# Optimization experiments

Measured on AMD Instinct MI355X. Metric: run time of the kernel, lower is better.

The kernel has to match this reference:

```python
import jax, jax.numpy as jnp
import numpy as np

N = 50000
EPS = 1e-16


def _gat_conv(x, w, att_src, att_dst, bias, src, dst, heads, out_ch, concat):
    # x: [N, F_in]; w: [heads*out_ch, F_in]; att_*: [heads, out_ch]; bias: [heads*out_ch] or [out_ch]
    n = x.shape[0]
    xw = (x @ w.T).reshape(n, heads, out_ch)              # [N, H, C]
    a_src = jnp.einsum('nhc,hc->nh', xw, att_src)          # [N, H]
    a_dst = jnp.einsum('nhc,hc->nh', xw, att_dst)
    alpha = a_src[src] + a_dst[dst]                        # [E, H]
    alpha = jax.nn.leaky_relu(alpha, negative_slope=0.2)
    # segment softmax over destination node (every node has a self loop)
    m = jax.ops.segment_max(alpha, dst, num_segments=n)    # [N, H]
    e = jnp.exp(alpha - m[dst])
    s = jax.ops.segment_sum(e, dst, num_segments=n)        # [N, H]
    coef = e / (s[dst] + EPS)                              # [E, H]
    out = jax.ops.segment_sum(xw[src] * coef[:, :, None], dst, num_segments=n)  # [N, H, C]
    if concat:
        out = out.reshape(n, heads * out_ch)
    else:
        out = out.mean(axis=1)
    return out + bias


def setup_inputs() -> dict:
    key = jax.random.key(0)
    ks = jax.random.split(key, 8)
    F_in, H, C1, NC = 128, 2, 64, 16
    E = 1_600_000
    x = jax.random.normal(ks[0], (N, F_in), dtype=jnp.float32)
    edge_index = jax.random.randint(ks[1], (2, E), 0, N, dtype=jnp.int64)
    w1 = jax.random.normal(ks[2], (H * C1, F_in), dtype=jnp.float32) / np.sqrt(F_in)
    att_src1 = jax.random.normal(ks[3], (H, C1), dtype=jnp.float32) / np.sqrt(C1)
    att_dst1 = jax.random.normal(ks[4], (H, C1), dtype=jnp.float32) / np.sqrt(C1)
    b1 = jnp.zeros((H * C1,), dtype=jnp.float32)
    w2 = jax.random.normal(ks[5], (NC, H * C1), dtype=jnp.float32) / np.sqrt(H * C1)
    att_src2 = jax.random.normal(ks[6], (1, NC), dtype=jnp.float32) / np.sqrt(NC)
    att_dst2 = jax.random.normal(ks[7], (1, NC), dtype=jnp.float32) / np.sqrt(NC)
    b2 = jnp.zeros((NC,), dtype=jnp.float32)
    return {"x": x, "edge_index": edge_index, "w1": w1, "att_src1": att_src1,
            "att_dst1": att_dst1, "b1": b1, "w2": w2, "att_src2": att_src2,
            "att_dst2": att_dst2, "b2": b2}


def reference(x, edge_index, w1, att_src1, att_dst1, b1, w2, att_src2, att_dst2, b2):
    n = x.shape[0]
    loop = jnp.arange(n, dtype=edge_index.dtype)
    src = jnp.concatenate([edge_index[0], loop])  # PyG adds self loops by default
    dst = jnp.concatenate([edge_index[1], loop])
    h = _gat_conv(x, w1, att_src1, att_dst1, b1, src, dst, heads=2, out_ch=64, concat=True)
    h = jax.nn.relu(h)
    # dropout p=0.5 is identity in eval mode
    out = _gat_conv(h, w2, att_src2, att_dst2, b2, src, dst, heads=1, out_ch=16, concat=True)
    return out
```

## Files before the change

kernel.cpp:

```cpp
#include <hip/hip_runtime.h>
#include <hip/hip_fp16.h>


#define BSHIFT 7
#define MAXB 512
#define CAPMAX 6144
#define XS 136

using f16x8 = __attribute__((ext_vector_type(8))) _Float16;
using f16x4 = __attribute__((ext_vector_type(4))) _Float16;
using f32x4 = __attribute__((ext_vector_type(4))) float;

__device__ __forceinline__ float lrelu(float a) { return fmaxf(a, 0.2f * a); }


__global__ __launch_bounds__(256) void part_gemm1_kernel(
    const int* __restrict__ src, const int* __restrict__ dst,
    int* __restrict__ bincur, unsigned* __restrict__ binned,
    int E, int B, int CH, int CAP, int NB,
    const float* __restrict__ x, const float* __restrict__ w1,
    const float* __restrict__ as1, const float* __restrict__ ad1,
    __half* __restrict__ xw1h, float* __restrict__ asrc1,
    float* __restrict__ adst1, int N) {
  __shared__ __align__(16) char smem[(64 + 128) * XS * 2];
  int t = threadIdx.x;

  if (blockIdx.x < (unsigned)NB) {
    int* s_h = (int*)smem;
    int* s_base = s_h + MAXB;
    int* s_cur = s_base + MAXB;
    unsigned* s_pack = (unsigned*)(s_cur + MAXB);
    for (int i = t; i < B; i += 256) s_h[i] = 0;
    __syncthreads();
    int lo = blockIdx.x * CH;
    int cnt = min(CH, E - lo);
    for (int i = t; i < cnt; i += 256) {
      int d = dst[lo + i];
      int s = src[lo + i];
      atomicAdd(&s_h[d >> BSHIFT], 1);
      s_pack[i] = (unsigned)s | ((unsigned)(d & 127) << 16) |
                  ((unsigned)(d >> BSHIFT) << 23);
    }
    __syncthreads();
    for (int i = t; i < B; i += 256) {
      int c = s_h[i];
      s_base[i] = c ? (i * CAP + atomicAdd(&bincur[i], c)) : 0;
      s_cur[i] = 0;
    }
    __syncthreads();
    for (int i = t; i < cnt; i += 256) {
      unsigned e = s_pack[i];
      int b = e >> 23;
      int r = atomicAdd(&s_cur[b], 1);
      binned[s_base[b] + r] = e & 0x7FFFFFu;
    }
    return;
  }

  _Float16* lx = (_Float16*)smem;
  _Float16* lw = lx + 64 * XS;
  int n0 = (blockIdx.x - NB) * 64;

#pragma unroll
  for (int j = 0; j < 8; ++j) {
    int idx = t + 256 * j;
    int nd = idx >> 5, i4 = (idx & 31) * 4;
    int gn = n0 + nd;
    float4 v = (gn < N) ? *(const float4*)&x[(size_t)gn * 128 + i4]
                        : make_float4(0.f, 0.f, 0.f, 0.f);
    f16x4 h;
    h[0] = (_Float16)v.x; h[1] = (_Float16)v.y;
    h[2] = (_Float16)v.z; h[3] = (_Float16)v.w;
    *(f16x4*)&lx[nd * XS + i4] = h;
  }
#pragma unroll
  for (int j = 0; j < 16; ++j) {
    int idx = t + 256 * j;
    int o = idx >> 5, i4 = (idx & 31) * 4;
    float4 v = *(const float4*)&w1[(size_t)o * 128 + i4];
    f16x4 h;
    h[0] = (_Float16)v.x; h[1] = (_Float16)v.y;
    h[2] = (_Float16)v.z; h[3] = (_Float16)v.w;
    *(f16x4*)&lw[o * XS + i4] = h;
  }
  __syncthreads();

  int lane = t & 63, wv = t >> 6;
  int m16 = lane & 15, q = lane >> 4;

  f32x4 acc[8];
#pragma unroll
  for (int i = 0; i < 8; ++i) acc[i] = (f32x4){0.f, 0.f, 0.f, 0.f};

#pragma unroll
  for (int c = 0; c < 4; ++c) {
    f16x8 a = *(const f16x8*)&lx[(16 * wv + m16) * XS + c * 32 + q * 8];
#pragma unroll
    for (int tt = 0; tt < 8; ++tt) {
      f16x8 b = *(const f16x8*)&lw[(tt * 16 + m16) * XS + c * 32 + q * 8];
      acc[tt] = __builtin_amdgcn_mfma_f32_16x16x32_f16(a, b, acc[tt], 0, 0, 0);
    }
  }

#pragma unroll
  for (int tt = 0; tt < 8; ++tt) {
#pragma unroll
    for (int r = 0; r < 4; ++r) {
      lx[(16 * wv + 4 * q + r) * XS + tt * 16 + m16] = (_Float16)acc[tt][r];
    }
  }

  {
    float ps = 0.f, pd = 0.f;
    int p = q;
#pragma unroll
    for (int k = 0; k < 4; ++k) {
      f16x8 hv = *(const f16x8*)&lx[(16 * wv + m16) * XS + p * 32 + k * 8];
      float4 s0 = *(const float4*)&as1[p * 32 + k * 8];
      float4 s1 = *(const float4*)&as1[p * 32 + k * 8 + 4];
      float4 d0 = *(const float4*)&ad1[p * 32 + k * 8];
      float4 d1 = *(const float4*)&ad1[p * 32 + k * 8 + 4];
      ps += (float)hv[0] * s0.x + (float)hv[1] * s0.y + (float)hv[2] * s0.z +
            (float)hv[3] * s0.w + (float)hv[4] * s1.x + (float)hv[5] * s1.y +
            (float)hv[6] * s1.z + (float)hv[7] * s1.w;
      pd += (float)hv[0] * d0.x + (float)hv[1] * d0.y + (float)hv[2] * d0.z +
            (float)hv[3] * d0.w + (float)hv[4] * d1.x + (float)hv[5] * d1.y +
            (float)hv[6] * d1.z + (float)hv[7] * d1.w;
    }
    ps += __shfl_xor(ps, 16);
    pd += __shfl_xor(pd, 16);
    int n = n0 + 16 * wv + m16;
    if (n < N && (q == 0 || q == 2)) {
      int hh = q >> 1;
      asrc1[2 * n + hh] = ps;
      adst1[2 * n + hh] = pd;
    }
  }

#pragma unroll
  for (int i = 0; i < 4; ++i) {
    int m = q + 4 * i;
    int n = n0 + 16 * wv + m;
    if (n < N) {
      uint4 v = *(const uint4*)&lx[(16 * wv + m) * XS + m16 * 8];
      *(uint4*)&xw1h[(size_t)n * 128 + m16 * 8] = v;
    }
  }
}


__global__ __launch_bounds__(256) void bucket_build_kernel(const unsigned* __restrict__ binned,
                                                           const int* __restrict__ bincur,
                                                           int2* __restrict__ nodeseg,
                                                           unsigned short* __restrict__ csr,
                                                           int N, int CAP) {
  __shared__ int s_deg[128];
  __shared__ int s_cur[128];
  __shared__ int s_wsum;
  __shared__ unsigned s_edges[CAPMAX];
  int b = blockIdx.x;
  int lo = b * CAP, hi = lo + bincur[b];
  int cnt = hi - lo;
  int t = threadIdx.x;
  if (t < 128) s_deg[t] = 0;
  int stg = min(cnt, CAPMAX);
  for (int i = t; i < stg; i += 256) s_edges[i] = binned[lo + i];
  __syncthreads();
  for (int i = t; i < cnt; i += 256) {
    unsigned e = (i < CAPMAX) ? s_edges[i] : binned[lo + i];
    atomicAdd(&s_deg[e >> 16], 1);
  }
  __syncthreads();
  int lane = t & 63, wv = t >> 6;
  int v = (t < 128) ? s_deg[t] : 0;
  int incl = v;
#pragma unroll
  for (int off = 1; off < 64; off <<= 1) {
    int u = __shfl_up(incl, off);
    if (lane >= off) incl += u;
  }
  if (t == 63) s_wsum = incl;
  __syncthreads();
  int excl = incl - v + ((wv == 1) ? s_wsum : 0);
  if (t < 128) {
    int node = (b << BSHIFT) + t;
    if (node < N) nodeseg[node] = make_int2(lo + excl, lo + excl + v);
    s_cur[t] = lo + excl;
  }
  __syncthreads();
  for (int i = t; i < cnt; i += 256) {
    unsigned e = (i < CAPMAX) ? s_edges[i] : binned[lo + i];
    int p = atomicAdd(&s_cur[e >> 16], 1);
    csr[p] = (unsigned short)(e & 0xFFFFu);
  }
}


__global__ __launch_bounds__(256) void agg1h_kernel(const __half* __restrict__ xw1h,
                                                    const float* __restrict__ asrc1,
                                                    const float* __restrict__ adst1,
                                                    const float* __restrict__ b1,
                                                    const float* __restrict__ w2,
                                                    const unsigned short* __restrict__ csr,
                                                    const int2* __restrict__ nodeseg,
                                                    float* __restrict__ p_out, int N) {
  __shared__ int s_off[4][64];
  __shared__ float s_w[4][64];
  int lane = threadIdx.x & 63, wv = threadIdx.x >> 6;
  int head = blockIdx.x & 1;
  int d = (blockIdx.x >> 1) * 4 + wv;
  if (d >= N) return;
  int c8 = lane & 7;
  int row = lane >> 3;
  int2 seg = nodeseg[d];
  int e0 = seg.x, e1 = seg.y;
  float adv = adst1[2 * d + head];
  float wself = __expf(lrelu(asrc1[2 * d + head] + adv));

  const char* xb = (const char*)xw1h + (head << 7) + 16 * c8;

  float a[8];
  float sum = 0.f;
#pragma unroll
  for (int k = 0; k < 8; ++k) a[k] = 0.f;
  if (row == 0) {
    uint4 r = *(const uint4*)(xb + ((size_t)d << 8));
    const __half2* hp = (const __half2*)&r;
#pragma unroll
    for (int k = 0; k < 4; ++k) {
      float2 v = __half22float2(hp[k]);
      a[2 * k] = wself * v.x;
      a[2 * k + 1] = wself * v.y;
    }
    sum = wself;
  }

  for (int base = e0; base < e1; base += 64) {
    int cnt = min(64, e1 - base);
    if (lane < cnt) {
      int s = (int)csr[base + lane];
      s_off[wv][lane] = s << 8;
      s_w[wv][lane] = __expf(lrelu(asrc1[2 * s + head] + adv));
    }
    int j = 0;
    for (; j + 15 < cnt; j += 16) {
      int oA = s_off[wv][j + row];
      int oB = s_off[wv][j + 8 + row];
      float wA = s_w[wv][j + row];
      float wB = s_w[wv][j + 8 + row];
      uint4 rA = *(const uint4*)(xb + oA);
      uint4 rB = *(const uint4*)(xb + oB);
      const __half2* hA = (const __half2*)&rA;
      const __half2* hB = (const __half2*)&rB;
#pragma unroll
      for (int k = 0; k < 4; ++k) {
        float2 vA = __half22float2(hA[k]);
        float2 vB = __half22float2(hB[k]);
        a[2 * k] += wA * vA.x + wB * vB.x;
        a[2 * k + 1] += wA * vA.y + wB * vB.y;
      }
      sum += wA + wB;
    }
    for (; j + 7 < cnt; j += 8) {
      int oA = s_off[wv][j + row];
      float wA = s_w[wv][j + row];
      uint4 rA = *(const uint4*)(xb + oA);
      const __half2* hA = (const __half2*)&rA;
#pragma unroll
      for (int k = 0; k < 4; ++k) {
        float2 vA = __half22float2(hA[k]);
        a[2 * k] += wA * vA.x;
        a[2 * k + 1] += wA * vA.y;
      }
      sum += wA;
    }
    if (row < cnt - j) {
      int oA = s_off[wv][j + row];
      float wA = s_w[wv][j + row];
      uint4 rA = *(const uint4*)(xb + oA);
      const __half2* hA = (const __half2*)&rA;
#pragma unroll
      for (int k = 0; k < 4; ++k) {
        float2 vA = __half22float2(hA[k]);
        a[2 * k] += wA * vA.x;
        a[2 * k + 1] += wA * vA.y;
      }
      sum += wA;
    }
  }

#pragma unroll
  for (int k = 0; k < 8; ++k) {
    a[k] += __shfl_xor(a[k], 8);
    a[k] += __shfl_xor(a[k], 16);
    a[k] += __shfl_xor(a[k], 32);
  }
  sum += __shfl_xor(sum, 8);
  sum += __shfl_xor(sum, 16);
  sum += __shfl_xor(sum, 32);

  float inv = 1.f / (sum + 1e-16f);
  int cb = head * 64 + 8 * c8;
  float4 blo = *(const float4*)&b1[cb];
  float4 bhi = *(const float4*)&b1[cb + 4];
  float h[8];
  h[0] = fmaxf(a[0] * inv + blo.x, 0.f);
  h[1] = fmaxf(a[1] * inv + blo.y, 0.f);
  h[2] = fmaxf(a[2] * inv + blo.z, 0.f);
  h[3] = fmaxf(a[3] * inv + blo.w, 0.f);
  h[4] = fmaxf(a[4] * inv + bhi.x, 0.f);
  h[5] = fmaxf(a[5] * inv + bhi.y, 0.f);
  h[6] = fmaxf(a[6] * inv + bhi.z, 0.f);
  h[7] = fmaxf(a[7] * inv + bhi.w, 0.f);

  float p0, p1;
  {
    const float* wr0 = &w2[(size_t)(2 * row) * 128 + cb];
    const float* wr1 = &w2[(size_t)(2 * row + 1) * 128 + cb];
    float4 w0lo = *(const float4*)wr0;
    float4 w0hi = *(const float4*)(wr0 + 4);
    float4 w1lo = *(const float4*)wr1;
    float4 w1hi = *(const float4*)(wr1 + 4);
    p0 = h[0] * w0lo.x + h[1] * w0lo.y + h[2] * w0lo.z + h[3] * w0lo.w +
         h[4] * w0hi.x + h[5] * w0hi.y + h[6] * w0hi.z + h[7] * w0hi.w;
    p1 = h[0] * w1lo.x + h[1] * w1lo.y + h[2] * w1lo.z + h[3] * w1lo.w +
         h[4] * w1hi.x + h[5] * w1hi.y + h[6] * w1hi.z + h[7] * w1hi.w;
  }
#pragma unroll
  for (int k = 1; k < 8; k <<= 1) {
    p0 += __shfl_xor(p0, k);
    p1 += __shfl_xor(p1, k);
  }
  if (c8 == 0) {
    *(float2*)&p_out[(size_t)d * 32 + head * 16 + 2 * row] =
        make_float2(p0, p1);
  }
}


__global__ __launch_bounds__(256) void combine_kernel(const float* __restrict__ p,
                                                      const float* __restrict__ as2,
                                                      const float* __restrict__ ad2,
                                                      __half* __restrict__ xw2h,
                                                      float* __restrict__ asrc2,
                                                      float* __restrict__ adst2, int N) {
  int idx = blockIdx.x * 256 + threadIdx.x;
  int node = idx >> 4, c = idx & 15;
  if (node >= N) return;
  float v = p[(size_t)node * 32 + c] + p[(size_t)node * 32 + 16 + c];
  xw2h[(size_t)node * 16 + c] = __float2half(v);
  float qs = v * as2[c], qd = v * ad2[c];
#pragma unroll
  for (int k = 1; k < 16; k <<= 1) {
    qs += __shfl_xor(qs, k);
    qd += __shfl_xor(qd, k);
  }
  if (c == 0) {
    asrc2[node] = qs;
    adst2[node] = qd;
  }
}


__global__ __launch_bounds__(256) void agg2_kernel(const __half* __restrict__ xw2h,
                                                   const float* __restrict__ asrc2,
                                                   const float* __restrict__ adst2,
                                                   const float* __restrict__ b2,
                                                   const unsigned short* __restrict__ csr,
                                                   const int2* __restrict__ nodeseg,
                                                   float* __restrict__ out, int N) {
  __shared__ int s_off[4][64];
  __shared__ float s_w[4][64];
  int lane = threadIdx.x & 63, wv = threadIdx.x >> 6;
  int d = blockIdx.x * 4 + wv;
  if (d >= N) return;
  int c2 = lane & 7;
  int row = lane >> 3;
  int2 seg = nodeseg[d];
  int e0 = seg.x, e1 = seg.y;
  float advd = adst2[d];
  float wself = __expf(lrelu(asrc2[d] + advd));
  const char* xb = (const char*)xw2h + 4 * c2;

  float a0 = 0.f, a1 = 0.f, sum = 0.f;
  if (row == 0) {
    float2 v = __half22float2(*(const __half2*)(xb + (size_t)d * 32));
    a0 = wself * v.x;
    a1 = wself * v.y;
    sum = wself;
  }
  for (int base = e0; base < e1; base += 64) {
    int cnt = min(64, e1 - base);
    if (lane < cnt) {
      int s = (int)csr[base + lane];
      s_off[wv][lane] = s << 5;
      s_w[wv][lane] = __expf(lrelu(asrc2[s] + advd));
    }
    int j = 0;
    for (; j + 15 < cnt; j += 16) {
      int o0 = s_off[wv][j + row];
      int o1 = s_off[wv][j + 8 + row];
      float w0 = s_w[wv][j + row];
      float w1 = s_w[wv][j + 8 + row];
      float2 v0 = __half22float2(*(const __half2*)(xb + o0));
      float2 v1 = __half22float2(*(const __half2*)(xb + o1));
      a0 += w0 * v0.x + w1 * v1.x;
      a1 += w0 * v0.y + w1 * v1.y;
      sum += w0 + w1;
    }
    for (; j + 7 < cnt; j += 8) {
      int o0 = s_off[wv][j + row];
      float w0 = s_w[wv][j + row];
      float2 v0 = __half22float2(*(const __half2*)(xb + o0));
      a0 += w0 * v0.x;
      a1 += w0 * v0.y;
      sum += w0;
    }
    if (row < cnt - j) {
      int o0 = s_off[wv][j + row];
      float w0 = s_w[wv][j + row];
      float2 v0 = __half22float2(*(const __half2*)(xb + o0));
      a0 += w0 * v0.x;
      a1 += w0 * v0.y;
      sum += w0;
    }
  }
#pragma unroll
  for (int k = 8; k < 64; k <<= 1) {
    a0 += __shfl_xor(a0, k);
    a1 += __shfl_xor(a1, k);
    sum += __shfl_xor(sum, k);
  }
  if (lane < 8) {
    float inv = 1.f / (sum + 1e-16f);
    float2 r;
    r.x = a0 * inv + b2[2 * c2];
    r.y = a1 * inv + b2[2 * c2 + 1];
    *(float2*)&out[(size_t)d * 16 + 2 * c2] = r;
  }
}


extern "C" void kernel_launch(void* const* d_in, const int* in_sizes, int n_in,
                              void* d_out, int out_size, void* d_ws, size_t ws_size,
                              hipStream_t stream) {
  const float* x = (const float*)d_in[0];
  const int* ei = (const int*)d_in[1];
  const float* w1 = (const float*)d_in[2];
  const float* as1 = (const float*)d_in[3];
  const float* ad1 = (const float*)d_in[4];
  const float* b1 = (const float*)d_in[5];
  const float* w2 = (const float*)d_in[6];
  const float* as2 = (const float*)d_in[7];
  const float* ad2 = (const float*)d_in[8];
  const float* b2 = (const float*)d_in[9];
  float* out = (float*)d_out;

  int N = in_sizes[0] / 128;
  int E = in_sizes[1] / 2;
  const int* srcp = ei;
  const int* dstp = ei + E;

  int B = (N + (1 << BSHIFT) - 1) >> BSHIFT;
  int mean = (E + B - 1) / B;
  int CAP = (mean + mean / 4 + 512 + 255) & ~255;
  const int NB = 256;
  int CH = (E + NB - 1) / NB;
  int GB = (N + 63) / 64;

  char* p = (char*)d_ws;
  auto alloc = [&](size_t bytes) -> void* {
    void* r = (void*)p;
    p += (bytes + 255) & ~(size_t)255;
    return r;
  };
  __half* xw1h = (__half*)alloc((size_t)N * 128 * 2);
  float* asrc1 = (float*)alloc((size_t)N * 2 * 4);
  float* adst1 = (float*)alloc((size_t)N * 2 * 4);
  __half* xw2h = (__half*)alloc((size_t)N * 16 * 2);
  float* asrc2 = (float*)alloc((size_t)N * 4);
  float* adst2 = (float*)alloc((size_t)N * 4);
  float* p_out = (float*)alloc((size_t)N * 32 * 4);
  int2* nodeseg = (int2*)alloc((size_t)N * 8);
  unsigned short* csr = (unsigned short*)alloc((size_t)B * CAP * 2);
  unsigned* binned = (unsigned*)alloc((size_t)B * CAP * 4);
  int* bincur = (int*)alloc((size_t)B * 4);

  hipMemsetAsync(bincur, 0, (size_t)B * 4, stream);
  part_gemm1_kernel<<<NB + GB, 256, 0, stream>>>(srcp, dstp, bincur, binned,
                                                 E, B, CH, CAP, NB,
                                                 x, w1, as1, ad1, xw1h, asrc1, adst1, N);
  bucket_build_kernel<<<B, 256, 0, stream>>>(binned, bincur, nodeseg, csr, N, CAP);
  agg1h_kernel<<<2 * ((N + 3) / 4), 256, 0, stream>>>(xw1h, asrc1, adst1, b1, w2,
                                                      csr, nodeseg, p_out, N);
  combine_kernel<<<(N * 16 + 255) / 256, 256, 0, stream>>>(p_out, as2, ad2,
                                                           xw2h, asrc2, adst2, N);
  agg2_kernel<<<(N + 3) / 4, 256, 0, stream>>>(xw2h, asrc2, adst2, b2, csr, nodeseg, out, N);
}
```

Baseline: 215.6 us.

## Aggregate layer-1 per 32-node bucket quarter with block-staged edge lists

```diff
diff --git a/kernel.cpp b/kernel.cpp
--- a/kernel.cpp
+++ b/kernel.cpp
@@ -6,6 +6,8 @@
 #define MAXB 512
 #define CAPMAX 6144
 #define XS 136
+#define STGQ 1536
+#define QSH 5
 
 using f16x8 = __attribute__((ext_vector_type(8))) _Float16;
 using f16x4 = __attribute__((ext_vector_type(4))) _Float16;
@@ -196,7 +198,7 @@
 }
 
 
-__global__ __launch_bounds__(256) void agg1h_kernel(const __half* __restrict__ xw1h,
+__global__ __launch_bounds__(256) void agg1b_kernel(const __half* __restrict__ xw1h,
                                                     const float* __restrict__ asrc1,
                                                     const float* __restrict__ adst1,
                                                     const float* __restrict__ b1,
@@ -204,136 +206,151 @@
                                                     const unsigned short* __restrict__ csr,
                                                     const int2* __restrict__ nodeseg,
                                                     float* __restrict__ p_out, int N) {
-  __shared__ int s_off[4][64];
-  __shared__ float s_w[4][64];
-  int lane = threadIdx.x & 63, wv = threadIdx.x >> 6;
+  __shared__ int s_off[STGQ];
+  __shared__ float s_al[STGQ];
+  __shared__ int2 s_seg[32];
+  __shared__ float s_ad[32];
+  __shared__ float s_as[32];
+
+  int t = threadIdx.x;
   int head = blockIdx.x & 1;
-  int d = (blockIdx.x >> 1) * 4 + wv;
-  if (d >= N) return;
+  int quarter = (blockIdx.x >> 1) & 3;
+  int bucket = blockIdx.x >> 3;
+  int n0 = (bucket << BSHIFT) + (quarter << QSH);
+  int nCnt = min(32, N - n0);
+  if (nCnt <= 0) return;
+
+  int lo = nodeseg[n0].x;
+  int hi = nodeseg[n0 + nCnt - 1].y;
+  int cnt = hi - lo;
+
+  if (t < nCnt) {
+    int2 sg = nodeseg[n0 + t];
+    s_seg[t] = make_int2(sg.x - lo, sg.y - lo);
+    s_ad[t] = adst1[2 * (n0 + t) + head];
+    s_as[t] = asrc1[2 * (n0 + t) + head];
+  }
+#pragma unroll
+  for (int kk = 0; kk < STGQ / 256; ++kk) {
+    int i = t + 256 * kk;
+    if (i < cnt) {
+      int s = (int)csr[lo + i];
+      s_off[i] = s << 8;
+      s_al[i] = asrc1[2 * s + head];
+    }
+  }
+  __syncthreads();
+
+  int lane = t & 63, wv = t >> 6;
   int c8 = lane & 7;
   int row = lane >> 3;
-  int2 seg = nodeseg[d];
-  int e0 = seg.x, e1 = seg.y;
-  float adv = adst1[2 * d + head];
-  float wself = __expf(lrelu(asrc1[2 * d + head] + adv));
-
   const char* xb = (const char*)xw1h + (head << 7) + 16 * c8;
 
-  float a[8];
-  float sum = 0.f;
-#pragma unroll
-  for (int k = 0; k < 8; ++k) a[k] = 0.f;
-  if (row == 0) {
-    uint4 r = *(const uint4*)(xb + ((size_t)d << 8));
-    const __half2* hp = (const __half2*)&r;
-#pragma unroll
-    for (int k = 0; k < 4; ++k) {
-      float2 v = __half22float2(hp[k]);
-      a[2 * k] = wself * v.x;
-      a[2 * k + 1] = wself * v.y;
-    }
-    sum = wself;
-  }
-
-  for (int base = e0; base < e1; base += 64) {
-    int cnt = min(64, e1 - base);
-    if (lane < cnt) {
-      int s = (int)csr[base + lane];
-      s_off[wv][lane] = s << 8;
-      s_w[wv][lane] = __expf(lrelu(asrc1[2 * s + head] + adv));
-    }
-    int j = 0;
-    for (; j + 15 < cnt; j += 16) {
-      int oA = s_off[wv][j + row];
-      int oB = s_off[wv][j + 8 + row];
-      float wA = s_w[wv][j + row];
-      float wB = s_w[wv][j + 8 + row];
-      uint4 rA = *(const uint4*)(xb + oA);
-      uint4 rB = *(const uint4*)(xb + oB);
-      const __half2* hA = (const __half2*)&rA;
-      const __half2* hB = (const __half2*)&rB;
-#pragma unroll
-      for (int k = 0; k < 4; ++k) {
-        float2 vA = __half22float2(hA[k]);
-        float2 vB = __half22float2(hB[k]);
-        a[2 * k] += wA * vA.x + wB * vB.x;
-        a[2 * k + 1] += wA * vA.y + wB * vB.y;
-      }
-      sum += wA + wB;
-    }
-    for (; j + 7 < cnt; j += 8) {
-      int oA = s_off[wv][j + row];
-      float wA = s_w[wv][j + row];
-      uint4 rA = *(const uint4*)(xb + oA);
-      const __half2* hA = (const __half2*)&rA;
-#pragma unroll
-      for (int k = 0; k < 4; ++k) {
-        float2 vA = __half22float2(hA[k]);
-        a[2 * k] += wA * vA.x;
-        a[2 * k + 1] += wA * vA.y;
-      }
-      sum += wA;
-    }
-    if (row < cnt - j) {
-      int oA = s_off[wv][j + row];
-      float wA = s_w[wv][j + row];
-      uint4 rA = *(const uint4*)(xb + oA);
-      const __half2* hA = (const __half2*)&rA;
-#pragma unroll
-      for (int k = 0; k < 4; ++k) {
-        float2 vA = __half22float2(hA[k]);
-        a[2 * k] += wA * vA.x;
-        a[2 * k + 1] += wA * vA.y;
-      }
-      sum += wA;
-    }
-  }
-
-#pragma unroll
-  for (int k = 0; k < 8; ++k) {
-    a[k] += __shfl_xor(a[k], 8);
-    a[k] += __shfl_xor(a[k], 16);
-    a[k] += __shfl_xor(a[k], 32);
-  }
-  sum += __shfl_xor(sum, 8);
-  sum += __shfl_xor(sum, 16);
-  sum += __shfl_xor(sum, 32);
-
-  float inv = 1.f / (sum + 1e-16f);
   int cb = head * 64 + 8 * c8;
   float4 blo = *(const float4*)&b1[cb];
   float4 bhi = *(const float4*)&b1[cb + 4];
-  float h[8];
-  h[0] = fmaxf(a[0] * inv + blo.x, 0.f);
-  h[1] = fmaxf(a[1] * inv + blo.y, 0.f);
-  h[2] = fmaxf(a[2] * inv + blo.z, 0.f);
-  h[3] = fmaxf(a[3] * inv + blo.w, 0.f);
-  h[4] = fmaxf(a[4] * inv + bhi.x, 0.f);
-  h[5] = fmaxf(a[5] * inv + bhi.y, 0.f);
-  h[6] = fmaxf(a[6] * inv + bhi.z, 0.f);
-  h[7] = fmaxf(a[7] * inv + bhi.w, 0.f);
-
-  float p0, p1;
-  {
-    const float* wr0 = &w2[(size_t)(2 * row) * 128 + cb];
-    const float* wr1 = &w2[(size_t)(2 * row + 1) * 128 + cb];
-    float4 w0lo = *(const float4*)wr0;
-    float4 w0hi = *(const float4*)(wr0 + 4);
-    float4 w1lo = *(const float4*)wr1;
-    float4 w1hi = *(const float4*)(wr1 + 4);
-    p0 = h[0] * w0lo.x + h[1] * w0lo.y + h[2] * w0lo.z + h[3] * w0lo.w +
-         h[4] * w0hi.x + h[5] * w0hi.y + h[6] * w0hi.z + h[7] * w0hi.w;
-    p1 = h[0] * w1lo.x + h[1] * w1lo.y + h[2] * w1lo.z + h[3] * w1lo.w +
-         h[4] * w1hi.x + h[5] * w1hi.y + h[6] * w1hi.z + h[7] * w1hi.w;
-  }
-#pragma unroll
-  for (int k = 1; k < 8; k <<= 1) {
-    p0 += __shfl_xor(p0, k);
-    p1 += __shfl_xor(p1, k);
-  }
-  if (c8 == 0) {
-    *(float2*)&p_out[(size_t)d * 32 + head * 16 + 2 * row] =
-        make_float2(p0, p1);
+  float4 w0lo = *(const float4*)&w2[(size_t)(2 * row) * 128 + cb];
+  float4 w0hi = *(const float4*)&w2[(size_t)(2 * row) * 128 + cb + 4];
+  float4 w1lo = *(const float4*)&w2[(size_t)(2 * row + 1) * 128 + cb];
+  float4 w1hi = *(const float4*)&w2[(size_t)(2 * row + 1) * 128 + cb + 4];
+
+  for (int nl = wv; nl < nCnt; nl += 4) {
+    int d = n0 + nl;
+    int2 sg = s_seg[nl];
+    float adv = s_ad[nl];
+    float wself = __expf(lrelu(s_as[nl] + adv));
+
+    float a[8];
+    float sum = 0.f;
+#pragma unroll
+    for (int k = 0; k < 8; ++k) a[k] = 0.f;
+    if (row == 0) {
+      uint4 r = *(const uint4*)(xb + ((size_t)d << 8));
+      const __half2* hp = (const __half2*)&r;
+#pragma unroll
+      for (int k = 0; k < 4; ++k) {
+        float2 v = __half22float2(hp[k]);
+        a[2 * k] = wself * v.x;
+        a[2 * k + 1] = wself * v.y;
+      }
+      sum = wself;
+    }
+
+    for (int base = sg.x; base < sg.y; base += 64) {
+      int take = sg.y - base;
+      if (take > 64) take = 64;
+      uint4 rr[8];
+      float wgt[8];
+#pragma unroll
+      for (int k = 0; k < 8; ++k) {
+        int e = row + 8 * k;
+        if (e < take) {
+          int idx = base + e;
+          int off;
+          float al;
+          if (idx < STGQ) {
+            off = s_off[idx];
+            al = s_al[idx];
+          } else {
+            int s = (int)csr[lo + idx];
+            off = s << 8;
+            al = asrc1[2 * s + head];
+          }
+          rr[k] = *(const uint4*)(xb + off);
+          wgt[k] = __expf(lrelu(al + adv));
+        }
+      }
+#pragma unroll
+      for (int k = 0; k < 8; ++k) {
+        int e = row + 8 * k;
+        if (e < take) {
+          const __half2* hp = (const __half2*)&rr[k];
+          float w = wgt[k];
+#pragma unroll
+          for (int q2 = 0; q2 < 4; ++q2) {
+            float2 v = __half22float2(hp[q2]);
+            a[2 * q2] += w * v.x;
+            a[2 * q2 + 1] += w * v.y;
+          }
+          sum += w;
+        }
+      }
+    }
+
+#pragma unroll
+    for (int k = 0; k < 8; ++k) {
+      a[k] += __shfl_xor(a[k], 8);
+      a[k] += __shfl_xor(a[k], 16);
+      a[k] += __shfl_xor(a[k], 32);
+    }
+    sum += __shfl_xor(sum, 8);
+    sum += __shfl_xor(sum, 16);
+    sum += __shfl_xor(sum, 32);
+
+    float inv = 1.f / (sum + 1e-16f);
+    float h[8];
+    h[0] = fmaxf(a[0] * inv + blo.x, 0.f);
+    h[1] = fmaxf(a[1] * inv + blo.y, 0.f);
+    h[2] = fmaxf(a[2] * inv + blo.z, 0.f);
+    h[3] = fmaxf(a[3] * inv + blo.w, 0.f);
+    h[4] = fmaxf(a[4] * inv + bhi.x, 0.f);
+    h[5] = fmaxf(a[5] * inv + bhi.y, 0.f);
+    h[6] = fmaxf(a[6] * inv + bhi.z, 0.f);
+    h[7] = fmaxf(a[7] * inv + bhi.w, 0.f);
+
+    float p0 = h[0] * w0lo.x + h[1] * w0lo.y + h[2] * w0lo.z + h[3] * w0lo.w +
+               h[4] * w0hi.x + h[5] * w0hi.y + h[6] * w0hi.z + h[7] * w0hi.w;
+    float p1 = h[0] * w1lo.x + h[1] * w1lo.y + h[2] * w1lo.z + h[3] * w1lo.w +
+               h[4] * w1hi.x + h[5] * w1hi.y + h[6] * w1hi.z + h[7] * w1hi.w;
+#pragma unroll
+    for (int k = 1; k < 8; k <<= 1) {
+      p0 += __shfl_xor(p0, k);
+      p1 += __shfl_xor(p1, k);
+    }
+    if (c8 == 0) {
+      *(float2*)&p_out[(size_t)d * 32 + head * 16 + 2 * row] =
+          make_float2(p0, p1);
+    }
   }
 }
 
@@ -491,8 +508,8 @@
                                                  E, B, CH, CAP, NB,
                                                  x, w1, as1, ad1, xw1h, asrc1, adst1, N);
   bucket_build_kernel<<<B, 256, 0, stream>>>(binned, bincur, nodeseg, csr, N, CAP);
-  agg1h_kernel<<<2 * ((N + 3) / 4), 256, 0, stream>>>(xw1h, asrc1, adst1, b1, w2,
-                                                      csr, nodeseg, p_out, N);
+  agg1b_kernel<<<8 * B, 256, 0, stream>>>(xw1h, asrc1, adst1, b1, w2,
+                                          csr, nodeseg, p_out, N);
   combine_kernel<<<(N * 16 + 255) / 256, 256, 0, stream>>>(p_out, as2, ad2,
                                                            xw2h, asrc2, adst2, N);
   agg2_kernel<<<(N + 3) / 4, 256, 0, stream>>>(xw2h, asrc2, adst2, b2, csr, nodeseg, out, N);
```

Result: slower. 288.4 us (+33.8%).

## Precompute layer-2 edge attention weights in a separate kernel before aggregation

Applied to the files above, without the earlier changes.

```diff
diff --git a/kernel.cpp b/kernel.cpp
--- a/kernel.cpp
+++ b/kernel.cpp
@@ -153,6 +153,7 @@
                                                            const int* __restrict__ bincur,
                                                            int2* __restrict__ nodeseg,
                                                            unsigned short* __restrict__ csr,
+                                                           unsigned char* __restrict__ dstl,
                                                            int N, int CAP) {
   __shared__ int s_deg[128];
   __shared__ int s_cur[128];
@@ -192,6 +193,7 @@
     unsigned e = (i < CAPMAX) ? s_edges[i] : binned[lo + i];
     int p = atomicAdd(&s_cur[e >> 16], 1);
     csr[p] = (unsigned short)(e & 0xFFFFu);
+    dstl[p] = (unsigned char)((e >> 16) & 127u);
   }
 }
 
@@ -362,11 +364,28 @@
 }
 
 
+__global__ __launch_bounds__(256) void wprep2_kernel(const unsigned short* __restrict__ csr,
+                                                     const unsigned char* __restrict__ dstl,
+                                                     const int* __restrict__ bincur,
+                                                     const float* __restrict__ asrc2,
+                                                     const float* __restrict__ adst2,
+                                                     float* __restrict__ wexp2, int CAP) {
+  int b = blockIdx.y;
+  int slot = blockIdx.x * 256 + threadIdx.x;
+  if (slot >= bincur[b]) return;
+  int i = b * CAP + slot;
+  int s = (int)csr[i];
+  int d = (b << BSHIFT) + (int)dstl[i];
+  wexp2[i] = __expf(lrelu(asrc2[s] + adst2[d]));
+}
+
+
 __global__ __launch_bounds__(256) void agg2_kernel(const __half* __restrict__ xw2h,
                                                    const float* __restrict__ asrc2,
                                                    const float* __restrict__ adst2,
                                                    const float* __restrict__ b2,
                                                    const unsigned short* __restrict__ csr,
+                                                   const float* __restrict__ wexp2,
                                                    const int2* __restrict__ nodeseg,
                                                    float* __restrict__ out, int N) {
   __shared__ int s_off[4][64];
@@ -378,8 +397,7 @@
   int row = lane >> 3;
   int2 seg = nodeseg[d];
   int e0 = seg.x, e1 = seg.y;
-  float advd = adst2[d];
-  float wself = __expf(lrelu(asrc2[d] + advd));
+  float wself = __expf(lrelu(asrc2[d] + adst2[d]));
   const char* xb = (const char*)xw2h + 4 * c2;
 
   float a0 = 0.f, a1 = 0.f, sum = 0.f;
@@ -392,37 +410,27 @@
   for (int base = e0; base < e1; base += 64) {
     int cnt = min(64, e1 - base);
     if (lane < cnt) {
-      int s = (int)csr[base + lane];
-      s_off[wv][lane] = s << 5;
-      s_w[wv][lane] = __expf(lrelu(asrc2[s] + advd));
-    }
-    int j = 0;
-    for (; j + 15 < cnt; j += 16) {
-      int o0 = s_off[wv][j + row];
-      int o1 = s_off[wv][j + 8 + row];
-      float w0 = s_w[wv][j + row];
-      float w1 = s_w[wv][j + 8 + row];
-      float2 v0 = __half22float2(*(const __half2*)(xb + o0));
-      float2 v1 = __half22float2(*(const __half2*)(xb + o1));
-      a0 += w0 * v0.x + w1 * v1.x;
-      a1 += w0 * v0.y + w1 * v1.y;
-      sum += w0 + w1;
-    }
-    for (; j + 7 < cnt; j += 8) {
-      int o0 = s_off[wv][j + row];
-      float w0 = s_w[wv][j + row];
-      float2 v0 = __half22float2(*(const __half2*)(xb + o0));
-      a0 += w0 * v0.x;
-      a1 += w0 * v0.y;
-      sum += w0;
-    }
-    if (row < cnt - j) {
-      int o0 = s_off[wv][j + row];
-      float w0 = s_w[wv][j + row];
-      float2 v0 = __half22float2(*(const __half2*)(xb + o0));
-      a0 += w0 * v0.x;
-      a1 += w0 * v0.y;
-      sum += w0;
+      s_off[wv][lane] = ((int)csr[base + lane]) << 5;
+      s_w[wv][lane] = wexp2[base + lane];
+    }
+    float2 vv[8];
+    float ww[8];
+#pragma unroll
+    for (int k = 0; k < 8; ++k) {
+      int e = row + 8 * k;
+      if (e < cnt) {
+        vv[k] = __half22float2(*(const __half2*)(xb + s_off[wv][e]));
+        ww[k] = s_w[wv][e];
+      }
+    }
+#pragma unroll
+    for (int k = 0; k < 8; ++k) {
+      int e = row + 8 * k;
+      if (e < cnt) {
+        a0 += ww[k] * vv[k].x;
+        a1 += ww[k] * vv[k].y;
+        sum += ww[k];
+      }
     }
   }
 #pragma unroll
@@ -483,6 +491,8 @@
   float* p_out = (float*)alloc((size_t)N * 32 * 4);
   int2* nodeseg = (int2*)alloc((size_t)N * 8);
   unsigned short* csr = (unsigned short*)alloc((size_t)B * CAP * 2);
+  unsigned char* dstl = (unsigned char*)alloc((size_t)B * CAP);
+  float* wexp2 = (float*)alloc((size_t)B * CAP * 4);
   unsigned* binned = (unsigned*)alloc((size_t)B * CAP * 4);
   int* bincur = (int*)alloc((size_t)B * 4);
 
@@ -490,10 +500,13 @@
   part_gemm1_kernel<<<NB + GB, 256, 0, stream>>>(srcp, dstp, bincur, binned,
                                                  E, B, CH, CAP, NB,
                                                  x, w1, as1, ad1, xw1h, asrc1, adst1, N);
-  bucket_build_kernel<<<B, 256, 0, stream>>>(binned, bincur, nodeseg, csr, N, CAP);
+  bucket_build_kernel<<<B, 256, 0, stream>>>(binned, bincur, nodeseg, csr, dstl, N, CAP);
   agg1h_kernel<<<2 * ((N + 3) / 4), 256, 0, stream>>>(xw1h, asrc1, adst1, b1, w2,
                                                       csr, nodeseg, p_out, N);
   combine_kernel<<<(N * 16 + 255) / 256, 256, 0, stream>>>(p_out, as2, ad2,
                                                            xw2h, asrc2, adst2, N);
-  agg2_kernel<<<(N + 3) / 4, 256, 0, stream>>>(xw2h, asrc2, adst2, b2, csr, nodeseg, out, N);
-}
+  dim3 wg((CAP + 255) / 256, B);
+  wprep2_kernel<<<wg, 256, 0, stream>>>(csr, dstl, bincur, asrc2, adst2, wexp2, CAP);
+  agg2_kernel<<<(N + 3) / 4, 256, 0, stream>>>(xw2h, asrc2, adst2, b2, csr, wexp2,
+                                               nodeseg, out, N);
+}
```

New measurement: 226.0 us. +4.8%, slower.

## Pack layer-2 attention score with features into per-node records; split layer-1 asrc by head

Applied to the files above, without the earlier changes.

```diff
diff --git a/kernel.cpp b/kernel.cpp
--- a/kernel.cpp
+++ b/kernel.cpp
@@ -20,7 +20,7 @@
     int E, int B, int CH, int CAP, int NB,
     const float* __restrict__ x, const float* __restrict__ w1,
     const float* __restrict__ as1, const float* __restrict__ ad1,
-    __half* __restrict__ xw1h, float* __restrict__ asrc1,
+    __half* __restrict__ xw1h, float* __restrict__ asrc1h,
     float* __restrict__ adst1, int N) {
   __shared__ __align__(16) char smem[(64 + 128) * XS * 2];
   int t = threadIdx.x;
@@ -132,7 +132,7 @@
     int n = n0 + 16 * wv + m16;
     if (n < N && (q == 0 || q == 2)) {
       int hh = q >> 1;
-      asrc1[2 * n + hh] = ps;
+      asrc1h[hh * N + n] = ps;
       adst1[2 * n + hh] = pd;
     }
   }
@@ -197,7 +197,7 @@
 
 
 __global__ __launch_bounds__(256) void agg1h_kernel(const __half* __restrict__ xw1h,
-                                                    const float* __restrict__ asrc1,
+                                                    const float* __restrict__ asrc1h,
                                                     const float* __restrict__ adst1,
                                                     const float* __restrict__ b1,
                                                     const float* __restrict__ w2,
@@ -214,8 +214,9 @@
   int row = lane >> 3;
   int2 seg = nodeseg[d];
   int e0 = seg.x, e1 = seg.y;
+  const float* asp = asrc1h + (size_t)head * N;
   float adv = adst1[2 * d + head];
-  float wself = __expf(lrelu(asrc1[2 * d + head] + adv));
+  float wself = __expf(lrelu(asp[d] + adv));
 
   const char* xb = (const char*)xw1h + (head << 7) + 16 * c8;
 
@@ -240,7 +241,7 @@
     if (lane < cnt) {
       int s = (int)csr[base + lane];
       s_off[wv][lane] = s << 8;
-      s_w[wv][lane] = __expf(lrelu(asrc1[2 * s + head] + adv));
+      s_w[wv][lane] = __expf(lrelu(asp[s] + adv));
     }
     int j = 0;
     for (; j + 15 < cnt; j += 16) {
@@ -341,102 +342,102 @@
 __global__ __launch_bounds__(256) void combine_kernel(const float* __restrict__ p,
                                                       const float* __restrict__ as2,
                                                       const float* __restrict__ ad2,
-                                                      __half* __restrict__ xw2h,
-                                                      float* __restrict__ asrc2,
+                                                      char* __restrict__ rec2,
                                                       float* __restrict__ adst2, int N) {
   int idx = blockIdx.x * 256 + threadIdx.x;
   int node = idx >> 4, c = idx & 15;
   if (node >= N) return;
   float v = p[(size_t)node * 32 + c] + p[(size_t)node * 32 + 16 + c];
-  xw2h[(size_t)node * 16 + c] = __float2half(v);
   float qs = v * as2[c], qd = v * ad2[c];
 #pragma unroll
   for (int k = 1; k < 16; k <<= 1) {
     qs += __shfl_xor(qs, k);
     qd += __shfl_xor(qd, k);
   }
+  char* rb = rec2 + (size_t)node * 64;
+  ((__half*)(rb + 4))[c] = __float2half(v);
   if (c == 0) {
-    asrc2[node] = qs;
+    *(float*)rb = qs;
     adst2[node] = qd;
   }
 }
 
 
-__global__ __launch_bounds__(256) void agg2_kernel(const __half* __restrict__ xw2h,
-                                                   const float* __restrict__ asrc2,
+__global__ __launch_bounds__(256) void agg2_kernel(const char* __restrict__ rec2,
                                                    const float* __restrict__ adst2,
                                                    const float* __restrict__ b2,
                                                    const unsigned short* __restrict__ csr,
                                                    const int2* __restrict__ nodeseg,
                                                    float* __restrict__ out, int N) {
   __shared__ int s_off[4][64];
-  __shared__ float s_w[4][64];
   int lane = threadIdx.x & 63, wv = threadIdx.x >> 6;
   int d = blockIdx.x * 4 + wv;
   if (d >= N) return;
-  int c2 = lane & 7;
-  int row = lane >> 3;
+  int sub = lane & 15;
+  int g = lane >> 4;
   int2 seg = nodeseg[d];
   int e0 = seg.x, e1 = seg.y;
   float advd = adst2[d];
-  float wself = __expf(lrelu(asrc2[d] + advd));
-  const char* xb = (const char*)xw2h + 4 * c2;
 
   float a0 = 0.f, a1 = 0.f, sum = 0.f;
-  if (row == 0) {
-    float2 v = __half22float2(*(const __half2*)(xb + (size_t)d * 32));
-    a0 = wself * v.x;
-    a1 = wself * v.y;
-    sum = wself;
-  }
+
+  if (g == 0) {
+    unsigned rv = *(const unsigned*)(rec2 + (size_t)d * 64 + 4 * sub);
+    float al = __uint_as_float(__shfl(rv, 0));
+    float w = __expf(lrelu(al + advd));
+    float2 v = __half22float2(*(const __half2*)&rv);
+    if (sub >= 1 && sub <= 8) {
+      a0 = w * v.x;
+      a1 = w * v.y;
+    } else if (sub == 0) {
+      sum = w;
+    }
+  }
+
   for (int base = e0; base < e1; base += 64) {
     int cnt = min(64, e1 - base);
-    if (lane < cnt) {
-      int s = (int)csr[base + lane];
-      s_off[wv][lane] = s << 5;
-      s_w[wv][lane] = __expf(lrelu(asrc2[s] + advd));
-    }
-    int j = 0;
-    for (; j + 15 < cnt; j += 16) {
-      int o0 = s_off[wv][j + row];
-      int o1 = s_off[wv][j + 8 + row];
-      float w0 = s_w[wv][j + row];
-      float w1 = s_w[wv][j + 8 + row];
-      float2 v0 = __half22float2(*(const __half2*)(xb + o0));
-      float2 v1 = __half22float2(*(const __half2*)(xb + o1));
-      a0 += w0 * v0.x + w1 * v1.x;
-      a1 += w0 * v0.y + w1 * v1.y;
-      sum += w0 + w1;
-    }
-    for (; j + 7 < cnt; j += 8) {
-      int o0 = s_off[wv][j + row];
-      float w0 = s_w[wv][j + row];
-      float2 v0 = __half22float2(*(const __half2*)(xb + o0));
-      a0 += w0 * v0.x;
-      a1 += w0 * v0.y;
-      sum += w0;
-    }
-    if (row < cnt - j) {
-      int o0 = s_off[wv][j + row];
-      float w0 = s_w[wv][j + row];
-      float2 v0 = __half22float2(*(const __half2*)(xb + o0));
-      a0 += w0 * v0.x;
-      a1 += w0 * v0.y;
-      sum += w0;
-    }
-  }
-#pragma unroll
-  for (int k = 8; k < 64; k <<= 1) {
-    a0 += __shfl_xor(a0, k);
-    a1 += __shfl_xor(a1, k);
-    sum += __shfl_xor(sum, k);
-  }
-  if (lane < 8) {
-    float inv = 1.f / (sum + 1e-16f);
+    if (lane < cnt) s_off[wv][lane] = ((int)csr[base + lane]) << 6;
+    for (int j = 0; j < cnt; j += 16) {
+      unsigned rv[4];
+#pragma unroll
+      for (int k = 0; k < 4; ++k) {
+        int e = j + 4 * k + g;
+        if (e < cnt) rv[k] = *(const unsigned*)(rec2 + s_off[wv][e] + 4 * sub);
+      }
+#pragma unroll
+      for (int k = 0; k < 4; ++k) {
+        int e = j + 4 * k + g;
+        if (e < cnt) {
+          float al = __uint_as_float(__shfl(rv[k], lane & 48));
+          float w = __expf(lrelu(al + advd));
+          float2 v = __half22float2(*(const __half2*)&rv[k]);
+          if (sub >= 1 && sub <= 8) {
+            a0 += w * v.x;
+            a1 += w * v.y;
+          } else if (sub == 0) {
+            sum += w;
+          }
+        }
+      }
+    }
+  }
+
+  a0 += __shfl_xor(a0, 16);
+  a0 += __shfl_xor(a0, 32);
+  a1 += __shfl_xor(a1, 16);
+  a1 += __shfl_xor(a1, 32);
+  sum += __shfl_xor(sum, 16);
+  sum += __shfl_xor(sum, 32);
+  float st = __shfl(sum, 0);
+
+  if (g == 0 && sub >= 1 && sub <= 8) {
+    int c0 = 2 * (sub - 1);
+    float inv = 1.f / (st + 1e-16f);
+    float2 bb = *(const float2*)&b2[c0];
     float2 r;
-    r.x = a0 * inv + b2[2 * c2];
-    r.y = a1 * inv + b2[2 * c2 + 1];
-    *(float2*)&out[(size_t)d * 16 + 2 * c2] = r;
+    r.x = a0 * inv + bb.x;
+    r.y = a1 * inv + bb.y;
+    *(float2*)&out[(size_t)d * 16 + c0] = r;
   }
 }
 
@@ -475,10 +476,9 @@
     return r;
   };
   __half* xw1h = (__half*)alloc((size_t)N * 128 * 2);
-  float* asrc1 = (float*)alloc((size_t)N * 2 * 4);
+  float* asrc1h = (float*)alloc((size_t)N * 2 * 4);
   float* adst1 = (float*)alloc((size_t)N * 2 * 4);
-  __half* xw2h = (__half*)alloc((size_t)N * 16 * 2);
-  float* asrc2 = (float*)alloc((size_t)N * 4);
+  char* rec2 = (char*)alloc((size_t)N * 64);
   float* adst2 = (float*)alloc((size_t)N * 4);
   float* p_out = (float*)alloc((size_t)N * 32 * 4);
   int2* nodeseg = (int2*)alloc((size_t)N * 8);
@@ -489,11 +489,11 @@
   hipMemsetAsync(bincur, 0, (size_t)B * 4, stream);
   part_gemm1_kernel<<<NB + GB, 256, 0, stream>>>(srcp, dstp, bincur, binned,
                                                  E, B, CH, CAP, NB,
-                                                 x, w1, as1, ad1, xw1h, asrc1, adst1, N);
+                                                 x, w1, as1, ad1, xw1h, asrc1h, adst1, N);
   bucket_build_kernel<<<B, 256, 0, stream>>>(binned, bincur, nodeseg, csr, N, CAP);
-  agg1h_kernel<<<2 * ((N + 3) / 4), 256, 0, stream>>>(xw1h, asrc1, adst1, b1, w2,
+  agg1h_kernel<<<2 * ((N + 3) / 4), 256, 0, stream>>>(xw1h, asrc1h, adst1, b1, w2,
                                                       csr, nodeseg, p_out, N);
   combine_kernel<<<(N * 16 + 255) / 256, 256, 0, stream>>>(p_out, as2, ad2,
-                                                           xw2h, asrc2, adst2, N);
-  agg2_kernel<<<(N + 3) / 4, 256, 0, stream>>>(xw2h, asrc2, adst2, b2, csr, nodeseg, out, N);
-}
+                                                           rec2, adst2, N);
+  agg2_kernel<<<(N + 3) / 4, 256, 0, stream>>>(rec2, adst2, b2, csr, nodeseg, out, N);
+}
```

New measurement: 218.7 us. No clear change (+1.5%).
